# Optimization experiments

Hardware: AMD Instinct MI355X
Metric: run time of the kernel (lower is better)

Reference implementation:

```python
import jax, jax.numpy as jnp
import numpy as np

BN_EPS = 1e-5


def setup_inputs() -> dict:
    key = jax.random.key(0)
    ks = jax.random.split(key, 9)
    b, c, h, w = 8, 256, 256, 25
    p2_r = jax.random.normal(ks[0], (b, c, h, w), dtype=jnp.float32)
    # message-passing conv weight; scaled so the 25-step recurrence stays bounded
    W_msg = jax.random.normal(ks[1], (256, 256, 1, 9), dtype=jnp.float32) * 0.02
    bn_gamma = jax.random.uniform(ks[2], (256,), dtype=jnp.float32, minval=0.5, maxval=1.5)
    bn_beta = jax.random.normal(ks[3], (256,), dtype=jnp.float32) * 0.1
    bn_mean = jax.random.normal(ks[4], (256,), dtype=jnp.float32) * 0.1
    bn_var = jax.random.uniform(ks[5], (256,), dtype=jnp.float32, minval=0.5, maxval=1.5)
    W_up2 = jax.random.normal(ks[6], (256, 256, 3, 3), dtype=jnp.float32) * (1.0 / np.sqrt(256 * 9))
    W_conv = jax.random.normal(ks[7], (1, 256, 1, 1), dtype=jnp.float32) * (1.0 / np.sqrt(256))
    W_conv2 = jax.random.normal(ks[8], (1, 25, 1, 1), dtype=jnp.float32) * (1.0 / np.sqrt(25))
    return {"p2_r": p2_r, "W_msg": W_msg, "bn_gamma": bn_gamma, "bn_beta": bn_beta,
            "bn_mean": bn_mean, "bn_var": bn_var, "W_up2": W_up2,
            "W_conv": W_conv, "W_conv2": W_conv2}


def r_scnn(x, Wc, reverse):
    # x: [b,c,h,w]. The (1,9) conv with padding (0,4) on width-1 slices only
    # touches the kernel's center tap -> per-step 256x256 matvec recurrence.
    xs = jnp.moveaxis(x, 3, 0)  # [w,b,c,h]
    if reverse:
        xs = xs[::-1]

    def step(carry, xi):
        new = xi + jax.nn.relu(jnp.einsum('oc,bch->boh', Wc, carry))
        return new, new

    _, rest = jax.lax.scan(step, xs[0], xs[1:])
    out = jnp.concatenate([xs[:1], rest], axis=0)[::-1]  # source reverses output order
    return jnp.moveaxis(out, 0, 3)  # [b,c,h,w]


def batchnorm(x, gamma, beta, mean, var):
    inv = gamma / jnp.sqrt(var + BN_EPS)
    return x * inv[None, :, None, None] + (beta - mean * inv)[None, :, None, None]


def upsample_h2(x):
    # bilinear, align_corners=True, size=(2H, W): only height doubles
    b, c, H, W = x.shape
    nh = 2 * H
    pos = jnp.arange(nh, dtype=jnp.float32) * ((H - 1) / (nh - 1))
    i0 = jnp.floor(pos).astype(jnp.int32)
    i1 = jnp.minimum(i0 + 1, H - 1)
    t = (pos - i0.astype(jnp.float32))[None, None, :, None]
    return x[:, :, i0, :] * (1.0 - t) + x[:, :, i1, :] * t


def reference(p2_r, W_msg, bn_gamma, bn_beta, bn_mean, bn_var, W_up2, W_conv, W_conv2):
    Wc = W_msg[:, :, 0, 4]  # effective center tap of the (1,9) conv
    x = r_scnn(p2_r, Wc, reverse=False)
    x = jax.nn.relu(batchnorm(x, bn_gamma, bn_beta, bn_mean, bn_var))
    x = r_scnn(x, Wc, reverse=True)
    x = jax.nn.relu(batchnorm(x, bn_gamma, bn_beta, bn_mean, bn_var))
    x = upsample_h2(x)  # [b,256,2h,w]
    x = jax.lax.conv_general_dilated(x, W_up2, (1, 1), ((1, 1), (1, 1)),
                                     dimension_numbers=('NCHW', 'OIHW', 'NCHW'))
    x = upsample_h2(x)  # [b,256,4h,w]
    x = jnp.einsum('oc,bchw->bohw', W_conv[:, :, 0, 0], x)  # 1x1 conv 256->1
    x = upsample_h2(x)  # [b,1,8h,w]
    x = jnp.swapaxes(x, 1, 3)  # [b,w,8h,1]
    x = jnp.einsum('oc,bchw->bohw', W_conv2[:, :, 0, 0], x)  # 1x1 conv 25->1
    return jax.nn.sigmoid(x)  # [b,1,8h,1]
```

## Files before the change

kernel.cpp:

```cpp
#include <hip/hip_runtime.h>
#include <math.h>


#define NC 8

typedef __attribute__((ext_vector_type(8))) short bf16x8;
typedef __attribute__((ext_vector_type(4))) float f32x4;

__device__ __forceinline__ float relu_(float v) { return fmaxf(v, 0.f); }

__device__ __forceinline__ short f2bf(float f) {
  union { float f; unsigned u; } v; v.f = f;
  unsigned r = (v.u + 0x7fffu + ((v.u >> 16) & 1u)) >> 16;
  return (short)r;
}
__device__ __forceinline__ float bf2f(short s) {
  union { unsigned u; float f; } v;
  v.u = ((unsigned)(unsigned short)s) << 16;
  return v.f;
}
__device__ __forceinline__ unsigned cvtpk(float lo, float hi) {
  unsigned r;
  asm("v_cvt_pk_bf16_f32 %0, %1, %2" : "=v"(r) : "v"(lo), "v"(hi));
  return r;
}

__global__ __launch_bounds__(64) void k0_precompute(
    const float* __restrict__ Wmsg, const float* __restrict__ gamma,
    const float* __restrict__ beta, const float* __restrict__ mean,
    const float* __restrict__ var, const float* __restrict__ Wup2,
    const float* __restrict__ Wconv, const float* __restrict__ Wconv2,
    short* __restrict__ WcA, float* __restrict__ A, float* __restrict__ bnp)
{
  const int c = blockIdx.x;
  const int lane = threadIdx.x;

  for (int o = lane; o < 256; o += 64)
    WcA[o * 256 + c] = f2bf(Wmsg[(o * 256 + c) * 9 + 4]);

  const int gtid = c * 64 + lane;
  if (gtid < 256) {
    float inv = gamma[gtid] / sqrtf(var[gtid] + 1e-5f);
    bnp[gtid] = inv;
    bnp[256 + gtid] = beta[gtid] - mean[gtid] * inv;
  }

  float wacc[9];
#pragma unroll
  for (int q = 0; q < 9; ++q) wacc[q] = 0.f;
  for (int o = lane; o < 256; o += 64) {
    float cw = Wconv[o];
    const float* wp = Wup2 + (size_t)(o * 256 + c) * 9;
#pragma unroll
    for (int q = 0; q < 9; ++q) wacc[q] += cw * wp[q];
  }
#pragma unroll
  for (int q = 0; q < 9; ++q) {
    float v = wacc[q];
    v += __shfl_xor(v, 32, 64);
    v += __shfl_xor(v, 16, 64);
    v += __shfl_xor(v, 8, 64);
    v += __shfl_xor(v, 4, 64);
    v += __shfl_xor(v, 2, 64);
    v += __shfl_xor(v, 1, 64);
    wacc[q] = v;
  }
  if (lane == 0) {
    for (int dh = 0; dh < 3; ++dh)
      for (int j = 0; j < 25; ++j) {
        float a = 0.f;
        for (int dw = 0; dw < 3; ++dw) {
          int w = j + 1 - dw;
          if (w >= 0 && w < 25) a += wacc[dh * 3 + dw] * Wconv2[w];
        }
        A[(dh * 25 + j) * 256 + c] = a;
      }
  }
}

__global__ __launch_bounds__(512) void k2_fused(
    const float* __restrict__ X,
    const short* __restrict__ WcA,
    const float* __restrict__ A,
    const float* __restrict__ bnp,
    float* __restrict__ S)
{
  __shared__ short xslab[25 * 8 * 256];
  __shared__ short yz[2][16 * 256];
  __shared__ float red[8][8][3];
  const int tid = threadIdx.x;
  const int wave = tid >> 6;
  const int lane = tid & 63;
  const int n = lane & 15;
  const int nr = n & 7;
  const int g = lane >> 4;
  const bool isz = (n >= 8);
  const int col0 = blockIdx.x * NC;
  const int b = col0 >> 8, h0 = col0 & 255;
  const int obase = wave * 32;
  char* xs = (char*)xslab;
  char* smem = (char*)yz;

  {
    const int L = lane;
    if (L < 50) {
      int base_[4], sx_[4];
#pragma unroll
      for (int e = 0; e < 4; ++e) {
        int f = 4 * L + e;
        int rn = f / 25, w = f - rn * 25;
        base_[e] = w * 4096 + rn * 512;
        sx_[e] = ((2 * rn + w) & 15) << 3;
      }
      const float* src0 = X + ((size_t)(b * 256 + obase) * 256 + h0) * 25 + 4 * L;
#pragma unroll
      for (int half = 0; half < 4; ++half) {
        float4 v[8];
#pragma unroll
        for (int i = 0; i < 8; ++i)
          v[i] = *(const float4*)(src0 + (size_t)(half * 8 + i) * 6400);
#pragma unroll
        for (int i = 0; i < 8; ++i) {
          int c2 = (obase + half * 8 + i) * 2;
          float vv[4] = {v[i].x, v[i].y, v[i].z, v[i].w};
#pragma unroll
          for (int e = 0; e < 4; ++e)
            *(short*)(xs + base_[e] + (c2 ^ sx_[e])) = f2bf(vv[e]);
        }
      }
    }
  }

  f32x4 inv[2], addv[2];
#pragma unroll
  for (int t = 0; t < 2; ++t) {
    inv[t] = *(const f32x4*)(bnp + obase + t * 16 + g * 4);
    addv[t] = *(const f32x4*)(bnp + 256 + obase + t * 16 + g * 4);
  }

  bf16x8 af[2][8];
#pragma unroll
  for (int t = 0; t < 2; ++t)
#pragma unroll
    for (int kk = 0; kk < 8; ++kk)
      af[t][kk] = *(const bf16x8*)(WcA + (obase + t * 16 + n) * 256 + kk * 32 + g * 8);

  const int swz = nr << 4;
  int woff[2], roff[8], xb[2];
#pragma unroll
  for (int t = 0; t < 2; ++t) {
    woff[t] = n * 512 + (((obase + t * 16 + g * 4) * 2) ^ swz);
    xb[t] = nr * 512 + 2 * (obase + t * 16 + g * 4);
  }
#pragma unroll
  for (int kk = 0; kk < 8; ++kk)
    roff[kk] = n * 512 + ((kk * 64 + g * 16) ^ swz);

  __syncthreads();

  {
    const int S0 = ((2 * nr) & 15) << 3;
    uint2 xq0[2];
#pragma unroll
    for (int t = 0; t < 2; ++t) xq0[t] = *(const uint2*)(xs + (xb[t] ^ S0));
    if (!isz) {
#pragma unroll
      for (int t = 0; t < 2; ++t)
        *(uint2*)(smem + woff[t]) = xq0[t];
    } else {
#pragma unroll
      for (int t = 0; t < 2; ++t) {
        float zr[4], t2r[4];
#pragma unroll
        for (int r = 0; r < 4; ++r) {
          short xbv = (short)(r < 2 ? (r ? (xq0[t].x >> 16) : xq0[t].x)
                                    : (r & 1 ? (xq0[t].y >> 16) : xq0[t].y));
          float x = bf2f(xbv);
          zr[r] = relu_(x * inv[t][r] + addv[t][r]);
          t2r[r] = relu_(zr[r] * inv[t][r] + addv[t][r]);
        }
        *(uint2*)(smem + woff[t]) = make_uint2(cvtpk(zr[0], zr[1]), cvtpk(zr[2], zr[3]));
        *(uint2*)(xs + (xb[t] ^ S0)) =
            make_uint2(cvtpk(t2r[0], t2r[1]), cvtpk(t2r[2], t2r[3]));
      }
    }
  }
  __syncthreads();

#pragma unroll 1
  for (int k = 1; k < 25; ++k) {
    const int cur = (k - 1) & 1, nxt = k & 1;
    const int Sk = ((2 * nr + k) & 15) << 3;
    const int kplane = k * 4096;

    uint2 xq[2];
    xq[0] = make_uint2(0u, 0u);
    xq[1] = make_uint2(0u, 0u);
    if (!isz) {
#pragma unroll
      for (int t = 0; t < 2; ++t)
        xq[t] = *(const uint2*)(xs + ((xb[t] + kplane) ^ Sk));
    }

    bf16x8 bfr[8];
#pragma unroll
    for (int kk = 0; kk < 8; ++kk)
      bfr[kk] = *(const bf16x8*)(smem + cur * 8192 + roff[kk]);

    f32x4 acc0a = (f32x4){0.f, 0.f, 0.f, 0.f};
    f32x4 acc0b = (f32x4){0.f, 0.f, 0.f, 0.f};
    f32x4 acc1a = (f32x4){0.f, 0.f, 0.f, 0.f};
    f32x4 acc1b = (f32x4){0.f, 0.f, 0.f, 0.f};
#pragma unroll
    for (int kk = 0; kk < 4; ++kk) {
      acc0a = __builtin_amdgcn_mfma_f32_16x16x32_bf16(af[0][kk], bfr[kk], acc0a, 0, 0, 0);
      acc1a = __builtin_amdgcn_mfma_f32_16x16x32_bf16(af[1][kk], bfr[kk], acc1a, 0, 0, 0);
    }
#pragma unroll
    for (int kk = 4; kk < 8; ++kk) {
      acc0b = __builtin_amdgcn_mfma_f32_16x16x32_bf16(af[0][kk], bfr[kk], acc0b, 0, 0, 0);
      acc1b = __builtin_amdgcn_mfma_f32_16x16x32_bf16(af[1][kk], bfr[kk], acc1b, 0, 0, 0);
    }
    f32x4 acc0 = acc0a + acc0b;
    f32x4 acc1 = acc1a + acc1b;

#pragma unroll
    for (int t = 0; t < 2; ++t) {
      f32x4 acc = t ? acc1 : acc0;
      float xv[4];
      xv[0] = bf2f((short)xq[t].x);
      xv[1] = bf2f((short)(xq[t].x >> 16));
      xv[2] = bf2f((short)xq[t].y);
      xv[3] = bf2f((short)(xq[t].y >> 16));
      float sel[4], tt2[4];
#pragma unroll
      for (int r = 0; r < 4; ++r) {
        float cy = relu_(acc[r]);
        float ynew = xv[r] + cy;
        float t1 = relu_(ynew * inv[t][r] + addv[t][r]);
        float t1s = __shfl_xor(t1, 8);
        float znew = t1s + cy;
        tt2[r] = relu_(znew * inv[t][r] + addv[t][r]);
        sel[r] = isz ? znew : ynew;
      }
      *(uint2*)(smem + nxt * 8192 + woff[t]) =
          make_uint2(cvtpk(sel[0], sel[1]), cvtpk(sel[2], sel[3]));
      if (isz)
        *(uint2*)(xs + ((xb[t] + kplane) ^ Sk)) =
            make_uint2(cvtpk(tt2[0], tt2[1]), cvtpk(tt2[2], tt2[3]));
    }
    __syncthreads();
  }

  {
    const int c = tid & 255;
    const int kh = tid >> 8;
    float acc[8][3];
#pragma unroll
    for (int nn = 0; nn < 8; ++nn)
#pragma unroll
      for (int dh = 0; dh < 3; ++dh) acc[nn][dh] = 0.f;

    const int kbeg = kh ? 13 : 0, kend = kh ? 25 : 13;
    for (int k = kbeg; k < kend; ++k) {
      float a0 = A[(0 * 25 + 24 - k) * 256 + c];
      float a1 = A[(1 * 25 + 24 - k) * 256 + c];
      float a2 = A[(2 * 25 + 24 - k) * 256 + c];
#pragma unroll
      for (int nn = 0; nn < 8; ++nn) {
        int Sp = ((2 * nn + k) & 15) << 3;
        float v = bf2f(*(const short*)(xs + ((k * 4096 + nn * 512 + 2 * c) ^ Sp)));
        acc[nn][0] = fmaf(a0, v, acc[nn][0]);
        acc[nn][1] = fmaf(a1, v, acc[nn][1]);
        acc[nn][2] = fmaf(a2, v, acc[nn][2]);
      }
    }
#pragma unroll
    for (int nn = 0; nn < 8; ++nn)
#pragma unroll
      for (int dh = 0; dh < 3; ++dh) {
        float v = acc[nn][dh];
        v += __shfl_xor(v, 1);
        v += __shfl_xor(v, 2);
        v += __shfl_xor(v, 4);
        v += __shfl_xor(v, 8);
        v += __shfl_xor(v, 16);
        v += __shfl_xor(v, 32);
        if (lane == 0) red[wave][nn][dh] = v;
      }
  }
  __syncthreads();
  if (tid < 24) {
    int nn = tid / 3, dh = tid % 3;
    float v = 0.f;
#pragma unroll
    for (int ww = 0; ww < 8; ++ww) v += red[ww][nn][dh];
    S[(size_t)(col0 + nn) * 3 + dh] = v;
  }
}

__global__ __launch_bounds__(256) void k3_outpre(
    const float* __restrict__ S, float* __restrict__ P)
{
  int idx = blockIdx.x * blockDim.x + threadIdx.x;
  if (idx >= 8 * 512) return;
  int b = idx >> 9, h = idx & 511;
  float acc = 0.f;
#pragma unroll
  for (int dh = 0; dh < 3; ++dh) {
    int hh = h + dh - 1;
    if (hh < 0 || hh >= 512) continue;
    float pos = hh * (255.0f / 511.0f);
    int i0 = (int)floorf(pos);
    int i1 = min(i0 + 1, 255);
    float t = pos - (float)i0;
    acc += (1.f - t) * S[(size_t)(b * 256 + i0) * 3 + dh]
         + t * S[(size_t)(b * 256 + i1) * 3 + dh];
  }
  P[idx] = acc;
}

__global__ __launch_bounds__(256) void k4_final(
    const float* __restrict__ P, float* __restrict__ out)
{
  int idx = blockIdx.x * blockDim.x + threadIdx.x;
  if (idx >= 8 * 2048) return;
  int b = idx >> 11, H = idx & 2047;
  const float* Pb = P + b * 512;

  float pos3 = H * (1023.0f / 2047.0f);
  int i3 = (int)floorf(pos3);
  int i3b = min(i3 + 1, 1023);
  float t3 = pos3 - (float)i3;

  float v[2];
#pragma unroll
  for (int q = 0; q < 2; ++q) {
    int i = q ? i3b : i3;
    float pos2 = i * (511.0f / 1023.0f);
    int i2 = (int)floorf(pos2);
    int i2b = min(i2 + 1, 511);
    float t2 = pos2 - (float)i2;
    v[q] = (1.f - t2) * Pb[i2] + t2 * Pb[i2b];
  }
  float val = (1.f - t3) * v[0] + t3 * v[1];
  out[idx] = 1.f / (1.f + expf(-val));
}

extern "C" void kernel_launch(void* const* d_in, const int* in_sizes, int n_in,
                              void* d_out, int out_size, void* d_ws, size_t ws_size,
                              hipStream_t stream) {
  (void)in_sizes; (void)n_in; (void)out_size; (void)ws_size;
  const float* p2r    = (const float*)d_in[0];
  const float* Wmsg   = (const float*)d_in[1];
  const float* gamma  = (const float*)d_in[2];
  const float* beta   = (const float*)d_in[3];
  const float* mean   = (const float*)d_in[4];
  const float* var    = (const float*)d_in[5];
  const float* Wup2   = (const float*)d_in[6];
  const float* Wconv  = (const float*)d_in[7];
  const float* Wconv2 = (const float*)d_in[8];
  float* out = (float*)d_out;

  float* ws = (float*)d_ws;
  size_t off = 0;
  short* WcA = (short*)(ws + off); off += 32768;
  float* Abuf = ws + off; off += 19200;
  float* bnp = ws + off;  off += 512;
  float* S = ws + off;    off += 6144;
  float* P = ws + off;    off += 4096;

  k0_precompute<<<256, 64, 0, stream>>>(Wmsg, gamma, beta, mean, var, Wup2,
                                        Wconv, Wconv2, WcA, Abuf, bnp);
  k2_fused<<<256, 512, 0, stream>>>(p2r, (const short*)WcA, Abuf, bnp, S);
  k3_outpre<<<16, 256, 0, stream>>>(S, P);
  k4_final<<<64, 256, 0, stream>>>(P, out);
}
```

Before: 58.04 us.

## Halve waves per block in fused recurrence kernel, each wave covering 64 channels

The fused scan kernel now runs 4 waves of 256 threads instead of 8, and each wave owns 64 output channels (4 MFMA tiles), so the per-step barrier synchronises fewer waves and each wave does more MFMA work between barriers. The input staging packs pairs of channels with a single packed bf16 conversion and does 32-bit LDS stores. The cross-lane xor-8 shuffle is replaced by a DPP row-rotate. The final reduction uses vectorised A loads and uint2 LDS reads split across the 4 waves. The cost is higher register pressure from 32 A fragments per wave and less parallelism per block during the serial 25-step recurrence.

```diff
diff --git a/kernel.cpp b/kernel.cpp
--- a/kernel.cpp
+++ b/kernel.cpp
@@ -23,6 +23,10 @@
   unsigned r;
   asm("v_cvt_pk_bf16_f32 %0, %1, %2" : "=v"(r) : "v"(lo), "v"(hi));
   return r;
+}
+__device__ __forceinline__ float dpp_xor8(float v) {
+  int r = __builtin_amdgcn_update_dpp(0, __float_as_int(v), 0x128, 0xf, 0xf, true);
+  return __int_as_float(r);
 }
 
 __global__ __launch_bounds__(64) void k0_precompute(
@@ -78,7 +82,7 @@
   }
 }
 
-__global__ __launch_bounds__(512) void k2_fused(
+__global__ __launch_bounds__(256, 1) void k2_fused(
     const float* __restrict__ X,
     const short* __restrict__ WcA,
     const float* __restrict__ A,
@@ -87,7 +91,7 @@
 {
   __shared__ short xslab[25 * 8 * 256];
   __shared__ short yz[2][16 * 256];
-  __shared__ float red[8][8][3];
+  __shared__ float red[4][8][3];
   const int tid = threadIdx.x;
   const int wave = tid >> 6;
   const int lane = tid & 63;
@@ -97,7 +101,7 @@
   const bool isz = (n >= 8);
   const int col0 = blockIdx.x * NC;
   const int b = col0 >> 8, h0 = col0 & 255;
-  const int obase = wave * 32;
+  const int obase = wave * 64;
   char* xs = (char*)xslab;
   char* smem = (char*)yz;
 
@@ -112,43 +116,39 @@
         base_[e] = w * 4096 + rn * 512;
         sx_[e] = ((2 * rn + w) & 15) << 3;
       }
-      const float* src0 = X + ((size_t)(b * 256 + obase) * 256 + h0) * 25 + 4 * L;
-#pragma unroll
-      for (int half = 0; half < 4; ++half) {
-        float4 v[8];
-#pragma unroll
-        for (int i = 0; i < 8; ++i)
-          v[i] = *(const float4*)(src0 + (size_t)(half * 8 + i) * 6400);
-#pragma unroll
-        for (int i = 0; i < 8; ++i) {
-          int c2 = (obase + half * 8 + i) * 2;
-          float vv[4] = {v[i].x, v[i].y, v[i].z, v[i].w};
-#pragma unroll
-          for (int e = 0; e < 4; ++e)
-            *(short*)(xs + base_[e] + (c2 ^ sx_[e])) = f2bf(vv[e]);
-        }
-      }
-    }
-  }
-
-  f32x4 inv[2], addv[2];
-#pragma unroll
-  for (int t = 0; t < 2; ++t) {
+      const float* src0 = X + (size_t)(b * 256 + obase) * 6400 + h0 * 25 + 4 * L;
+#pragma unroll 4
+      for (int i = 0; i < 32; ++i) {
+        float4 v0 = *(const float4*)(src0 + (size_t)(2 * i) * 6400);
+        float4 v1 = *(const float4*)(src0 + (size_t)(2 * i + 1) * 6400);
+        unsigned p[4] = {cvtpk(v0.x, v1.x), cvtpk(v0.y, v1.y),
+                         cvtpk(v0.z, v1.z), cvtpk(v0.w, v1.w)};
+        const int cb = 2 * obase + 4 * i;
+#pragma unroll
+        for (int e = 0; e < 4; ++e)
+          *(unsigned*)(xs + base_[e] + (cb ^ sx_[e])) = p[e];
+      }
+    }
+  }
+
+  f32x4 inv[4], addv[4];
+#pragma unroll
+  for (int t = 0; t < 4; ++t) {
     inv[t] = *(const f32x4*)(bnp + obase + t * 16 + g * 4);
     addv[t] = *(const f32x4*)(bnp + 256 + obase + t * 16 + g * 4);
   }
 
-  bf16x8 af[2][8];
-#pragma unroll
-  for (int t = 0; t < 2; ++t)
+  bf16x8 af[4][8];
+#pragma unroll
+  for (int t = 0; t < 4; ++t)
 #pragma unroll
     for (int kk = 0; kk < 8; ++kk)
       af[t][kk] = *(const bf16x8*)(WcA + (obase + t * 16 + n) * 256 + kk * 32 + g * 8);
 
   const int swz = nr << 4;
-  int woff[2], roff[8], xb[2];
-#pragma unroll
-  for (int t = 0; t < 2; ++t) {
+  int woff[4], xb[4], roff[8];
+#pragma unroll
+  for (int t = 0; t < 4; ++t) {
     woff[t] = n * 512 + (((obase + t * 16 + g * 4) * 2) ^ swz);
     xb[t] = nr * 512 + 2 * (obase + t * 16 + g * 4);
   }
@@ -160,23 +160,18 @@
 
   {
     const int S0 = ((2 * nr) & 15) << 3;
-    uint2 xq0[2];
-#pragma unroll
-    for (int t = 0; t < 2; ++t) xq0[t] = *(const uint2*)(xs + (xb[t] ^ S0));
-    if (!isz) {
-#pragma unroll
-      for (int t = 0; t < 2; ++t)
-        *(uint2*)(smem + woff[t]) = xq0[t];
-    } else {
-#pragma unroll
-      for (int t = 0; t < 2; ++t) {
+#pragma unroll
+    for (int t = 0; t < 4; ++t) {
+      uint2 xq0 = *(const uint2*)(xs + (xb[t] ^ S0));
+      if (!isz) {
+        *(uint2*)(smem + woff[t]) = xq0;
+      } else {
         float zr[4], t2r[4];
+        float xv[4] = {bf2f((short)xq0.x), bf2f((short)(xq0.x >> 16)),
+                       bf2f((short)xq0.y), bf2f((short)(xq0.y >> 16))};
 #pragma unroll
         for (int r = 0; r < 4; ++r) {
-          short xbv = (short)(r < 2 ? (r ? (xq0[t].x >> 16) : xq0[t].x)
-                                    : (r & 1 ? (xq0[t].y >> 16) : xq0[t].y));
-          float x = bf2f(xbv);
-          zr[r] = relu_(x * inv[t][r] + addv[t][r]);
+          zr[r] = relu_(xv[r] * inv[t][r] + addv[t][r]);
           t2r[r] = relu_(zr[r] * inv[t][r] + addv[t][r]);
         }
         *(uint2*)(smem + woff[t]) = make_uint2(cvtpk(zr[0], zr[1]), cvtpk(zr[2], zr[3]));
@@ -193,12 +188,12 @@
     const int Sk = ((2 * nr + k) & 15) << 3;
     const int kplane = k * 4096;
 
-    uint2 xq[2];
-    xq[0] = make_uint2(0u, 0u);
-    xq[1] = make_uint2(0u, 0u);
+    uint2 xq[4];
+#pragma unroll
+    for (int t = 0; t < 4; ++t) xq[t] = make_uint2(0u, 0u);
     if (!isz) {
 #pragma unroll
-      for (int t = 0; t < 2; ++t)
+      for (int t = 0; t < 4; ++t)
         xq[t] = *(const uint2*)(xs + ((xb[t] + kplane) ^ Sk));
     }
 
@@ -207,26 +202,26 @@
     for (int kk = 0; kk < 8; ++kk)
       bfr[kk] = *(const bf16x8*)(smem + cur * 8192 + roff[kk]);
 
-    f32x4 acc0a = (f32x4){0.f, 0.f, 0.f, 0.f};
-    f32x4 acc0b = (f32x4){0.f, 0.f, 0.f, 0.f};
-    f32x4 acc1a = (f32x4){0.f, 0.f, 0.f, 0.f};
-    f32x4 acc1b = (f32x4){0.f, 0.f, 0.f, 0.f};
-#pragma unroll
-    for (int kk = 0; kk < 4; ++kk) {
-      acc0a = __builtin_amdgcn_mfma_f32_16x16x32_bf16(af[0][kk], bfr[kk], acc0a, 0, 0, 0);
-      acc1a = __builtin_amdgcn_mfma_f32_16x16x32_bf16(af[1][kk], bfr[kk], acc1a, 0, 0, 0);
-    }
-#pragma unroll
-    for (int kk = 4; kk < 8; ++kk) {
-      acc0b = __builtin_amdgcn_mfma_f32_16x16x32_bf16(af[0][kk], bfr[kk], acc0b, 0, 0, 0);
-      acc1b = __builtin_amdgcn_mfma_f32_16x16x32_bf16(af[1][kk], bfr[kk], acc1b, 0, 0, 0);
-    }
-    f32x4 acc0 = acc0a + acc0b;
-    f32x4 acc1 = acc1a + acc1b;
-
-#pragma unroll
-    for (int t = 0; t < 2; ++t) {
-      f32x4 acc = t ? acc1 : acc0;
+    f32x4 accA[4], accB[4];
+#pragma unroll
+    for (int t = 0; t < 4; ++t) {
+      accA[t] = (f32x4){0.f, 0.f, 0.f, 0.f};
+      accB[t] = (f32x4){0.f, 0.f, 0.f, 0.f};
+    }
+#pragma unroll
+    for (int kk = 0; kk < 4; ++kk)
+#pragma unroll
+      for (int t = 0; t < 4; ++t)
+        accA[t] = __builtin_amdgcn_mfma_f32_16x16x32_bf16(af[t][kk], bfr[kk], accA[t], 0, 0, 0);
+#pragma unroll
+    for (int kk = 4; kk < 8; ++kk)
+#pragma unroll
+      for (int t = 0; t < 4; ++t)
+        accB[t] = __builtin_amdgcn_mfma_f32_16x16x32_bf16(af[t][kk], bfr[kk], accB[t], 0, 0, 0);
+
+#pragma unroll
+    for (int t = 0; t < 4; ++t) {
+      f32x4 acc = accA[t] + accB[t];
       float xv[4];
       xv[0] = bf2f((short)xq[t].x);
       xv[1] = bf2f((short)(xq[t].x >> 16));
@@ -238,7 +233,7 @@
         float cy = relu_(acc[r]);
         float ynew = xv[r] + cy;
         float t1 = relu_(ynew * inv[t][r] + addv[t][r]);
-        float t1s = __shfl_xor(t1, 8);
+        float t1s = dpp_xor8(t1);
         float znew = t1s + cy;
         tt2[r] = relu_(znew * inv[t][r] + addv[t][r]);
         sel[r] = isz ? znew : ynew;
@@ -253,48 +248,55 @@
   }
 
   {
-    const int c = tid & 255;
-    const int kh = tid >> 8;
+    const int kb = (wave == 0) ? 0 : 1 + 6 * wave;
+    const int ke = kb + (wave ? 6 : 7);
     float acc[8][3];
 #pragma unroll
-    for (int nn = 0; nn < 8; ++nn)
-#pragma unroll
-      for (int dh = 0; dh < 3; ++dh) acc[nn][dh] = 0.f;
-
-    const int kbeg = kh ? 13 : 0, kend = kh ? 25 : 13;
-    for (int k = kbeg; k < kend; ++k) {
-      float a0 = A[(0 * 25 + 24 - k) * 256 + c];
-      float a1 = A[(1 * 25 + 24 - k) * 256 + c];
-      float a2 = A[(2 * 25 + 24 - k) * 256 + c];
-#pragma unroll
-      for (int nn = 0; nn < 8; ++nn) {
-        int Sp = ((2 * nn + k) & 15) << 3;
-        float v = bf2f(*(const short*)(xs + ((k * 4096 + nn * 512 + 2 * c) ^ Sp)));
-        acc[nn][0] = fmaf(a0, v, acc[nn][0]);
-        acc[nn][1] = fmaf(a1, v, acc[nn][1]);
-        acc[nn][2] = fmaf(a2, v, acc[nn][2]);
-      }
-    }
-#pragma unroll
-    for (int nn = 0; nn < 8; ++nn)
+    for (int rn = 0; rn < 8; ++rn)
+#pragma unroll
+      for (int dh = 0; dh < 3; ++dh) acc[rn][dh] = 0.f;
+
+#pragma unroll 1
+    for (int k = kb; k < ke; ++k) {
+      f32x4 a0 = *(const f32x4*)(A + (0 * 25 + 24 - k) * 256 + 4 * lane);
+      f32x4 a1 = *(const f32x4*)(A + (1 * 25 + 24 - k) * 256 + 4 * lane);
+      f32x4 a2 = *(const f32x4*)(A + (2 * 25 + 24 - k) * 256 + 4 * lane);
+#pragma unroll
+      for (int rn = 0; rn < 8; ++rn) {
+        int Sp = ((2 * rn + k) & 15) << 3;
+        uint2 q = *(const uint2*)(xs + ((k * 4096 + rn * 512 + 8 * lane) ^ Sp));
+        float v0 = bf2f((short)q.x), v1 = bf2f((short)(q.x >> 16));
+        float v2 = bf2f((short)q.y), v3 = bf2f((short)(q.y >> 16));
+#pragma unroll
+        for (int dh = 0; dh < 3; ++dh) {
+          f32x4 a = dh == 0 ? a0 : (dh == 1 ? a1 : a2);
+          float s = acc[rn][dh];
+          s = fmaf(a[0], v0, s);
+          s = fmaf(a[1], v1, s);
+          s = fmaf(a[2], v2, s);
+          s = fmaf(a[3], v3, s);
+          acc[rn][dh] = s;
+        }
+      }
+    }
+#pragma unroll
+    for (int rn = 0; rn < 8; ++rn)
 #pragma unroll
       for (int dh = 0; dh < 3; ++dh) {
-        float v = acc[nn][dh];
+        float v = acc[rn][dh];
         v += __shfl_xor(v, 1);
         v += __shfl_xor(v, 2);
         v += __shfl_xor(v, 4);
         v += __shfl_xor(v, 8);
         v += __shfl_xor(v, 16);
         v += __shfl_xor(v, 32);
-        if (lane == 0) red[wave][nn][dh] = v;
+        if (lane == 0) red[wave][rn][dh] = v;
       }
   }
   __syncthreads();
   if (tid < 24) {
     int nn = tid / 3, dh = tid % 3;
-    float v = 0.f;
-#pragma unroll
-    for (int ww = 0; ww < 8; ++ww) v += red[ww][nn][dh];
+    float v = red[0][nn][dh] + red[1][nn][dh] + red[2][nn][dh] + red[3][nn][dh];
     S[(size_t)(col0 + nn) * 3 + dh] = v;
   }
 }
@@ -372,7 +374,7 @@
 
   k0_precompute<<<256, 64, 0, stream>>>(Wmsg, gamma, beta, mean, var, Wup2,
                                         Wconv, Wconv2, WcA, Abuf, bnp);
-  k2_fused<<<256, 512, 0, stream>>>(p2r, (const short*)WcA, Abuf, bnp, S);
+  k2_fused<<<256, 256, 0, stream>>>(p2r, (const short*)WcA, Abuf, bnp, S);
   k3_outpre<<<16, 256, 0, stream>>>(S, P);
   k4_final<<<64, 256, 0, stream>>>(P, out);
 }
```

Result: no change. 58.63 us (+1.0%).
